# Performance work log

Measured on AMD Instinct MI355X. Metric: run time of the kernel, lower is better.

## Reference

```python
import jax, jax.numpy as jnp
import numpy as np

N, NPG, BS = 32000, 1000, 32
E, H, L, R, K = 512000, 128, 3, 8, 64


def setup_inputs() -> dict:
    key = jax.random.key(0)
    ks = jax.random.split(key, 16)
    sc = 0.05
    x = jax.random.normal(ks[0], (N, H), jnp.float32)
    W_rel = jax.random.normal(ks[1], (L, R, H, H), jnp.float32) * sc
    W_self = jax.random.normal(ks[2], (L, H, H), jnp.float32) * sc
    rel_table = jax.random.normal(ks[3], (R, H), jnp.float32)
    Zn = jax.random.normal(ks[4], (K, H), jnp.float32) * sc
    proj_W = jax.random.normal(ks[5], (L * H, H), jnp.float32) * sc
    proj_b = jnp.zeros((H,), jnp.float32)
    fc_W = jax.random.normal(ks[6], (2 * L * H + 2 * H, 1), jnp.float32) * sc
    fc_b = jnp.zeros((1,), jnp.float32)
    rep_seq = jax.random.normal(ks[7], (BS, H), jnp.float32)
    src = jax.random.randint(ks[8], (E,), 0, N, jnp.int32)
    dst = jax.random.randint(ks[9], (E,), 0, N, jnp.int32)
    etype = jax.random.randint(ks[10], (E,), 0, R, jnp.int32)
    graph_id = (jnp.arange(N, dtype=jnp.int32) // NPG).astype(jnp.int32)
    head_ids = (jnp.arange(BS, dtype=jnp.int32) * NPG)           # node with id==1 per subgraph
    tail_ids = (jnp.arange(BS, dtype=jnp.int32) * NPG + 1)       # node with id==2 per subgraph
    rel_labels = jax.random.randint(ks[11], (BS,), 0, R, jnp.int32)
    return dict(x=x, W_rel=W_rel, W_self=W_self, rel_table=rel_table, Zn=Zn,
                proj_W=proj_W, proj_b=proj_b, fc_W=fc_W, fc_b=fc_b, rep_seq=rep_seq,
                src=src, dst=dst, etype=etype, graph_id=graph_id,
                head_ids=head_ids, tail_ids=tail_ids, rel_labels=rel_labels)


def reference(x, W_rel, W_self, rel_table, Zn, proj_W, proj_b, fc_W, fc_b, rep_seq,
              src, dst, etype, graph_id, head_ids, tail_ids, rel_labels):
    n, h_dim = x.shape
    bs = head_ids.shape[0]
    # RGCN message passing: aggregate src features per (dst, rel), then per-rel linear.
    seg = dst.astype(jnp.int32) * R + etype.astype(jnp.int32)  # [E]
    h = x
    reprs = []
    for l in range(L):
        agg = jax.ops.segment_sum(h[src], seg, num_segments=n * R)  # [N*R, H]
        agg = agg.reshape(n, R, h_dim)
        msg = jnp.einsum('nri,rio->no', agg, W_rel[l])
        h = jax.nn.relu(msg + h @ W_self[l])
        reprs.append(h)
    repr_ = jnp.stack(reprs, axis=1)  # [N, L, H]
    # mean_nodes pooling per subgraph
    counts = jax.ops.segment_sum(jnp.ones((n,), x.dtype), graph_id, num_segments=bs)
    g_mean = jax.ops.segment_sum(repr_, graph_id, num_segments=bs) / counts[:, None, None]
    g_out = jax.nn.leaky_relu(g_mean.reshape(bs, L * h_dim) @ proj_W + proj_b)  # [bs, H]
    # head/tail gathers
    head_flat = repr_[head_ids].reshape(bs, L * h_dim)
    tail_flat = repr_[tail_ids].reshape(bs, L * h_dim)
    rel_embs = rel_table[rel_labels]  # [bs, H]
    h_out = head_flat @ proj_W + proj_b
    t_out = tail_flat @ proj_W + proj_b
    # community view: cluster assignment (softmax) then summary (sigmoid)
    s1 = jax.nn.sigmoid(jax.nn.softmax(h_out @ Zn.T, axis=-1) @ Zn)
    s2 = jax.nn.sigmoid(jax.nn.softmax(t_out @ Zn.T, axis=-1) @ Zn)
    s = s1 * s2
    # view attention aggregation over [subgraph, sequence, community] views
    views = jnp.stack([g_out, rep_seq, s], axis=1)  # [bs, 3, H]
    att = jax.nn.softmax(jnp.sum(rel_embs[:, None, :] * views, axis=-1), axis=-1)  # [bs, 3]
    view_aggr = jnp.sum(att[:, :, None] * views, axis=1)  # [bs, H]
    # positive triplet scoring
    g_rep = jnp.concatenate([head_flat, tail_flat, rel_embs, view_aggr], axis=1)
    out_pos = g_rep @ fc_W + fc_b  # [bs, 1]
    return out_pos
```

## Files before the change

kernel.cpp:

```cpp
#include <hip/hip_runtime.h>

#define N_NODES 32000
#define NPG     1000
#define BSZ     32
#define NEDGE   512000
#define H       128
#define NL      3
#define NR      8
#define NKK     1152
#define NKA     1024
#define NBIN2   262144

typedef __attribute__((ext_vector_type(8))) short short8;
typedef __attribute__((ext_vector_type(4))) float float4v;

__device__ __forceinline__ float bf2f(unsigned short u) {
  union { unsigned int i; float f; } v;
  v.i = ((unsigned int)u) << 16;
  return v.f;
}
__device__ __forceinline__ unsigned short f2bf(float f) {
  union { float f; unsigned int i; } v;
  v.f = f;
  unsigned int x = v.i;
  return (unsigned short)((x + 0x7FFFu + ((x >> 16) & 1u)) >> 16);
}

__device__ __forceinline__ void gl_lds16(const void* g, void* l) {
  __builtin_amdgcn_global_load_lds((__attribute__((address_space(1))) void*)g,
                                   (__attribute__((address_space(3))) void*)l,
                                   16, 0, 0);
}

__global__ __launch_bounds__(256) void k_prep(
    const float* __restrict__ x, const float* __restrict__ W_rel,
    const float* __restrict__ W_self, const int* __restrict__ dst,
    const int* __restrict__ etype, const int* __restrict__ graph_id,
    unsigned short* __restrict__ hb, unsigned short* __restrict__ Bt,
    int* __restrict__ cnt, int* __restrict__ gcount)
{
  const int b = blockIdx.x, t = threadIdx.x;
  if (b < 4000) {
    const size_t i = ((size_t)b * 256 + t) * 4;
    float4 v = *(const float4*)(x + i);
    ushort4 u = { f2bf(v.x), f2bf(v.y), f2bf(v.z), f2bf(v.w) };
    *(ushort4*)(hb + i) = u;
  } else if (b < 5728) {
    const int g = (b - 4000) * 256 + t;
    const int l = g / (H * NKK);
    const int rem = g - l * (H * NKK);
    const int o = rem / NKK;
    const int kk = rem - o * NKK;
    float v = (kk < 1024)
        ? W_rel[(((size_t)l * NR + (kk >> 7)) * H + (kk & 127)) * H + o]
        : W_self[((size_t)l * H + (kk - 1024)) * H + o];
    Bt[g] = f2bf(v);
  } else if (b < 7728) {
    const int e = (b - 5728) * 256 + t;
    atomicAdd(&cnt[dst[e] * 8 + etype[e]], 1);
  } else {
    __shared__ int hist[BSZ];
    if (t < BSZ) hist[t] = 0;
    __syncthreads();
    const int n = (b - 7728) * 256 + t;
    if (n < N_NODES) atomicAdd(&hist[graph_id[n]], 1);
    __syncthreads();
    if (t < BSZ) { int v = hist[t]; if (v) atomicAdd(&gcount[t], v); }
  }
}

__global__ __launch_bounds__(256) void k_scanA(const int* __restrict__ cnt,
                                               int* __restrict__ bsum) {
  __shared__ int red[256];
  const int t = threadIdx.x;
  int4 v = *(const int4*)(cnt + blockIdx.x * 1024 + t * 4);
  red[t] = v.x + v.y + v.z + v.w;
  __syncthreads();
  for (int off = 128; off > 0; off >>= 1) {
    if (t < off) red[t] += red[t + off];
    __syncthreads();
  }
  if (t == 0) bsum[blockIdx.x] = red[0];
}

__global__ __launch_bounds__(256) void k_scanC(const int* __restrict__ cnt,
                                               const int* __restrict__ bsum,
                                               int* __restrict__ row_ptr2,
                                               int* __restrict__ cursor) {
  __shared__ int ts[256], bsx[256];
  const int t = threadIdx.x;
  const int base = blockIdx.x * 1024 + t * 4;
  int4 v = *(const int4*)(cnt + base);
  const int s = v.x + v.y + v.z + v.w;
  ts[t]  = s;
  bsx[t] = bsum[t];
  __syncthreads();
  for (int off = 1; off < 256; off <<= 1) {
    int a = (t >= off) ? ts[t - off]  : 0;
    int c = (t >= off) ? bsx[t - off] : 0;
    __syncthreads();
    ts[t] += a; bsx[t] += c;
    __syncthreads();
  }
  const int boff = (blockIdx.x == 0) ? 0 : bsx[blockIdx.x - 1];
  int ex = ts[t] - s + boff;
  int4 w = { ex, ex + v.x, ex + v.x + v.y, ex + v.x + v.y + v.z };
  *(int4*)(row_ptr2 + base) = w;
  *(int4*)(cursor + base) = w;
}

__global__ void k_fill(const int* __restrict__ src, const int* __restrict__ dst,
                       const int* __restrict__ etype, int* __restrict__ cursor,
                       int* __restrict__ edge_off) {
  int e = blockIdx.x * blockDim.x + threadIdx.x;
  if (e < NEDGE) {
    int p = atomicAdd(&cursor[dst[e] * 8 + etype[e]], 1);
    edge_off[p] = src[e];
  }
}

__global__ __launch_bounds__(256) void k_agg(
    const unsigned short* __restrict__ Hin,
    const int* __restrict__ row_ptr2,
    const int* __restrict__ edge_off,
    unsigned short* __restrict__ A)
{
  const int tid = threadIdx.x;
  const int j  = tid >> 5;
  const int li = tid & 31;
  const int p  = li >> 4;
  const int q  = li & 15;
  const int n  = blockIdx.x;
  const uint4* H4 = (const uint4*)Hin;
  const int b = row_ptr2[n * 8 + j];
  const int e = row_ptr2[n * 8 + j + 1];
  float acc[8] = {0.f, 0.f, 0.f, 0.f, 0.f, 0.f, 0.f, 0.f};
#define ACC8(u, ok) { \
    const unsigned int xx = (ok) ? (u).x : 0u, yy = (ok) ? (u).y : 0u; \
    const unsigned int zz = (ok) ? (u).z : 0u, ww = (ok) ? (u).w : 0u; \
    acc[0] += bf2f((unsigned short)(xx & 0xffff)); \
    acc[1] += bf2f((unsigned short)(xx >> 16));    \
    acc[2] += bf2f((unsigned short)(yy & 0xffff)); \
    acc[3] += bf2f((unsigned short)(yy >> 16));    \
    acc[4] += bf2f((unsigned short)(zz & 0xffff)); \
    acc[5] += bf2f((unsigned short)(zz >> 16));    \
    acc[6] += bf2f((unsigned short)(ww & 0xffff)); \
    acc[7] += bf2f((unsigned short)(ww >> 16)); }
  for (int k = b + p; k < e; k += 4) {
    const int k1 = k + 2;
    const bool v1 = k1 < e;
    const int o0 = edge_off[k];
    const int o1 = edge_off[v1 ? k1 : k];
    uint4 u0 = H4[(size_t)o0 * 16 + q];
    uint4 u1 = H4[(size_t)o1 * 16 + q];
    ACC8(u0, true)
    ACC8(u1, v1)
  }
#undef ACC8
  #pragma unroll
  for (int i = 0; i < 8; ++i) acc[i] += __shfl_xor(acc[i], 16);
  if (p == 0) {
    uint4 w;
    w.x = (unsigned int)f2bf(acc[0]) | ((unsigned int)f2bf(acc[1]) << 16);
    w.y = (unsigned int)f2bf(acc[2]) | ((unsigned int)f2bf(acc[3]) << 16);
    w.z = (unsigned int)f2bf(acc[4]) | ((unsigned int)f2bf(acc[5]) << 16);
    w.w = (unsigned int)f2bf(acc[6]) | ((unsigned int)f2bf(acc[7]) << 16);
    *(uint4*)(A + (size_t)n * NKA + j * H + q * 8) = w;
  }
}

__global__ __launch_bounds__(256, 3) void k_gemmA(
    const unsigned short* __restrict__ Ag,
    const unsigned short* __restrict__ Bg,
    const unsigned short* __restrict__ Hin,
    unsigned short* __restrict__ Hout,
    float* __restrict__ gmean, int layer)
{
  __shared__ __align__(16) unsigned short pool[24576];
  const int tid = threadIdx.x;
  const int w = tid >> 6, lane = tid & 63;
  const int l15 = lane & 15, quad = lane >> 4;
  const int m0 = blockIdx.x * 64;
  const int rbase = (w & 1) * 32;
  const int cbase = (w >> 1) * 64;

  float4v acc[2][4];
  #pragma unroll
  for (int i = 0; i < 2; ++i)
    #pragma unroll
    for (int jj = 0; jj < 4; ++jj) acc[i][jj] = (float4v){0.f, 0.f, 0.f, 0.f};

  auto stageA = [&](unsigned short* dstL, const int kb) {
    #pragma unroll
    for (int rep = 0; rep < 2; ++rep) {
      const int g = rep * 256 + tid, row = g >> 3, c = g & 7;
      const unsigned short* srcp = (kb < NKA)
          ? Ag  + (size_t)(m0 + row) * NKA + kb + ((c ^ (row & 7)) * 8)
          : Hin + (size_t)(m0 + row) * H + (kb - NKA) + ((c ^ (row & 7)) * 8);
      gl_lds16(srcp, dstL + (size_t)g * 8);
    }
  };
  auto stageB = [&](unsigned short* dstL, const int kb) {
    #pragma unroll
    for (int rep = 0; rep < 4; ++rep) {
      const int g = rep * 256 + tid, row = g >> 3, c = g & 7;
      gl_lds16(Bg + (size_t)row * NKK + kb + ((c ^ (row & 7)) * 8), dstL + (size_t)g * 8);
    }
  };

  stageA(pool, 0);
  stageB(pool + 4096, 0);
  __syncthreads();

  #pragma unroll 2
  for (int kt = 0; kt < 18; ++kt) {
    const int cur = kt & 1;
    const unsigned short* ac = pool + (cur ? 12288 : 0);
    const unsigned short* bc = pool + (cur ? 16384 : 4096);
    if (kt < 17) {
      const int kb = (kt + 1) * 64;
      stageA(pool + (cur ? 0 : 12288), kb);
      stageB(pool + (cur ? 4096 : 16384), kb);
    }
    #pragma unroll
    for (int s = 0; s < 2; ++s) {
      const int c = s * 4 + quad;
      short8 af[2], bfv[4];
      #pragma unroll
      for (int i = 0; i < 2; ++i) {
        const int row = rbase + i * 16 + l15;
        af[i] = *(const short8*)(ac + row * 64 + ((c ^ (row & 7)) * 8));
      }
      #pragma unroll
      for (int jj = 0; jj < 4; ++jj) {
        const int orow = cbase + jj * 16 + l15;
        bfv[jj] = *(const short8*)(bc + orow * 64 + ((c ^ (orow & 7)) * 8));
      }
      #pragma unroll
      for (int i = 0; i < 2; ++i)
        #pragma unroll
        for (int jj = 0; jj < 4; ++jj)
          acc[i][jj] = __builtin_amdgcn_mfma_f32_16x16x32_bf16(af[i], bfv[jj], acc[i][jj], 0, 0, 0);
    }
    __syncthreads();
  }

  #pragma unroll
  for (int i = 0; i < 2; ++i)
    #pragma unroll
    for (int jj = 0; jj < 4; ++jj)
      #pragma unroll
      for (int r = 0; r < 4; ++r) {
        const int row = rbase + i * 16 + quad * 4 + r;
        const int col = cbase + jj * 16 + l15;
        pool[row * 136 + col] = f2bf(fmaxf(acc[i][jj][r], 0.f));
      }
  __syncthreads();
  #pragma unroll
  for (int rep = 0; rep < 4; ++rep) {
    const int g = rep * 256 + tid;
    const int row = g >> 4, c = g & 15;
    *(uint4*)(Hout + (size_t)(m0 + row) * H + c * 8) = *(const uint4*)(pool + row * 136 + c * 8);
  }

  const int g0 = m0 / NPG;
  const int bnd = (g0 + 1) * NPG - m0;
  if (tid < H) {
    float s0 = 0.f, s1 = 0.f;
    #pragma unroll 8
    for (int r2 = 0; r2 < 64; ++r2) {
      float v = bf2f(pool[r2 * 136 + tid]);
      if (r2 < bnd) s0 += v; else s1 += v;
    }
    atomicAdd(&gmean[(size_t)g0 * (NL * H) + layer * H + tid], s0);
    if (bnd < 64)
      atomicAdd(&gmean[(size_t)(g0 + 1) * (NL * H) + layer * H + tid], s1);
  }
}

__global__ __launch_bounds__(128) void k_final(
    const unsigned short* __restrict__ hb, const float* __restrict__ gmean,
    const int* __restrict__ gcount,
    const float* __restrict__ rel_tb, const float* __restrict__ Zn,
    const float* __restrict__ projW, const float* __restrict__ projB,
    const float* __restrict__ fcW, const float* __restrict__ fcB,
    const float* __restrict__ repSeq,
    const int* __restrict__ head_ids, const int* __restrict__ tail_ids,
    const int* __restrict__ rel_lab, float* __restrict__ out)
{
  const int b = blockIdx.x;
  const int o = threadIdx.x;
  __shared__ float gm[384], hf[384], tf[384];
  __shared__ float go[128], ho[128], t_o[128], re[128], rs[128], sv[128];
  __shared__ float lg[128], pr[128], red[128], att[3];

  const int hid = head_ids[b], tlid = tail_ids[b], rl = rel_lab[b];
  const float cinv = 1.f / (float)gcount[b];
  #pragma unroll
  for (int l = 0; l < NL; ++l) {
    gm[l * H + o] = gmean[(size_t)b * (NL * H) + l * H + o] * cinv;
    hf[l * H + o] = bf2f(hb[((size_t)(l + 1) * N_NODES + hid) * H + o]);
    tf[l * H + o] = bf2f(hb[((size_t)(l + 1) * N_NODES + tlid) * H + o]);
  }
  re[o] = rel_tb[rl * H + o];
  rs[o] = repSeq[b * H + o];
  __syncthreads();

  float pb = projB[o];
  float sg = pb, sh = pb, st = pb;
  for (int i = 0; i < NL * H; ++i) {
    float wv = projW[i * H + o];
    sg = fmaf(gm[i], wv, sg);
    sh = fmaf(hf[i], wv, sh);
    st = fmaf(tf[i], wv, st);
  }
  go[o] = (sg > 0.f) ? sg : 0.01f * sg;
  ho[o] = sh;
  t_o[o] = st;
  __syncthreads();

  {
    const int k = o & 63;
    const float* v = (o < 64) ? ho : t_o;
    float s = 0.f;
    for (int i = 0; i < H; ++i) s = fmaf(v[i], Zn[k * H + i], s);
    lg[o] = s;
  }
  __syncthreads();
  if (o < 2) {
    float* l0 = &lg[o * 64];
    float* p0 = &pr[o * 64];
    float mx = l0[0];
    for (int k = 1; k < 64; ++k) mx = fmaxf(mx, l0[k]);
    float sum = 0.f;
    for (int k = 0; k < 64; ++k) { float e = __expf(l0[k] - mx); p0[k] = e; sum += e; }
    float inv = 1.f / sum;
    for (int k = 0; k < 64; ++k) p0[k] *= inv;
  }
  __syncthreads();
  {
    float s1 = 0.f, s2 = 0.f;
    for (int k = 0; k < 64; ++k) {
      float z = Zn[k * H + o];
      s1 = fmaf(pr[k], z, s1);
      s2 = fmaf(pr[64 + k], z, s2);
    }
    s1 = 1.f / (1.f + __expf(-s1));
    s2 = 1.f / (1.f + __expf(-s2));
    sv[o] = s1 * s2;
  }
  __syncthreads();
  if (o == 0) {
    float d0 = 0.f, d1 = 0.f, d2 = 0.f;
    for (int i = 0; i < H; ++i) { d0 += re[i] * go[i]; d1 += re[i] * rs[i]; d2 += re[i] * sv[i]; }
    float mx = fmaxf(d0, fmaxf(d1, d2));
    float e0 = __expf(d0 - mx), e1 = __expf(d1 - mx), e2 = __expf(d2 - mx);
    float inv = 1.f / (e0 + e1 + e2);
    att[0] = e0 * inv; att[1] = e1 * inv; att[2] = e2 * inv;
  }
  __syncthreads();
  float va = att[0] * go[o] + att[1] * rs[o] + att[2] * sv[o];

  float p = 0.f;
  p = fmaf(hf[o],       fcW[o],       p);
  p = fmaf(hf[128 + o], fcW[128 + o], p);
  p = fmaf(hf[256 + o], fcW[256 + o], p);
  p = fmaf(tf[o],       fcW[384 + o], p);
  p = fmaf(tf[128 + o], fcW[512 + o], p);
  p = fmaf(tf[256 + o], fcW[640 + o], p);
  p = fmaf(re[o],       fcW[768 + o], p);
  p = fmaf(va,          fcW[896 + o], p);
  red[o] = p;
  __syncthreads();
  if (o == 0) {
    float s = 0.f;
    for (int i = 0; i < 128; ++i) s += red[i];
    out[b] = s + fcB[0];
  }
}

extern "C" void kernel_launch(void* const* d_in, const int* in_sizes, int n_in,
                              void* d_out, int out_size, void* d_ws, size_t ws_size,
                              hipStream_t stream) {
  const float* x        = (const float*)d_in[0];
  const float* W_rel    = (const float*)d_in[1];
  const float* W_self   = (const float*)d_in[2];
  const float* rel_tb   = (const float*)d_in[3];
  const float* Zn       = (const float*)d_in[4];
  const float* proj_W   = (const float*)d_in[5];
  const float* proj_b   = (const float*)d_in[6];
  const float* fc_W     = (const float*)d_in[7];
  const float* fc_b     = (const float*)d_in[8];
  const float* rep_seq  = (const float*)d_in[9];
  const int* src      = (const int*)d_in[10];
  const int* dst      = (const int*)d_in[11];
  const int* etype    = (const int*)d_in[12];
  const int* graph_id = (const int*)d_in[13];
  const int* head_ids = (const int*)d_in[14];
  const int* tail_ids = (const int*)d_in[15];
  const int* rel_lab  = (const int*)d_in[16];
  float* out = (float*)d_out;

  char* w = (char*)d_ws;
  unsigned short* A   = (unsigned short*)w; w += (size_t)N_NODES * NKA * 2;
  unsigned short* hb  = (unsigned short*)w; w += (size_t)(NL + 1) * N_NODES * H * 2;
  unsigned short* Bt2 = (unsigned short*)w; w += (size_t)NL * H * NKK * 2;
  int* row_ptr2 = (int*)w;  w += (size_t)(NBIN2 + 8) * 4;
  int* cursor   = (int*)w;  w += (size_t)NBIN2 * 4;
  int* edge_off = (int*)w;  w += (size_t)NEDGE * 4;
  int* bsum     = (int*)w;  w += (size_t)256 * 4;
  char* z = w;
  int* cnt     = (int*)w;   w += (size_t)NBIN2 * 4;
  int* gcount  = (int*)w;   w += (size_t)32 * 4;
  float* gmean = (float*)w; w += (size_t)BSZ * NL * H * 4;
  size_t zbytes = (size_t)(w - z);

  hipMemsetAsync(z, 0, zbytes, stream);
  k_prep <<<7853, 256, 0, stream>>>(x, W_rel, W_self, dst, etype, graph_id, hb, Bt2, cnt, gcount);
  k_scanA<<<NBIN2 / 1024, 256, 0, stream>>>(cnt, bsum);
  k_scanC<<<NBIN2 / 1024, 256, 0, stream>>>(cnt, bsum, row_ptr2, cursor);
  k_fill <<<NEDGE / 256, 256, 0, stream>>>(src, dst, etype, cursor, edge_off);

  for (int l = 0; l < NL; ++l) {
    const unsigned short* hp = hb + (size_t)l * N_NODES * H;
    unsigned short* hn = hb + (size_t)(l + 1) * N_NODES * H;
    k_agg  <<<N_NODES, 256, 0, stream>>>(hp, row_ptr2, edge_off, A);
    k_gemmA<<<N_NODES / 64, 256, 0, stream>>>(A, Bt2 + (size_t)l * H * NKK, hp, hn, gmean, l);
  }
  k_final<<<BSZ, H, 0, stream>>>(hb, gmean, gcount, rel_tb, Zn, proj_W, proj_b, fc_W, fc_b,
                                 rep_seq, head_ids, tail_ids, rel_lab, out);
  (void)in_sizes; (void)n_in; (void)out_size; (void)ws_size;
}
```

Baseline: 333.3 us.

## Triple-buffer gemmA LDS pipeline with explicit vmcnt waits and nontemporal stores

Converts the k_gemmA main loop from double-buffered to triple-buffered LDS staging, prefetching two K-tiles ahead and using explicit s_waitcnt vmcnt counts with raw s_barrier instead of __syncthreads. This is meant to hide global-to-LDS load latency behind MFMA work. It raises LDS use to 72KB per block and lowers launch bounds occupancy from 3 to 2 blocks per CU. The aggregation kernel's output store also becomes a nontemporal vector store to reduce cache pollution.

Result: slower. 346.4 us (+3.9%).

```diff
diff --git a/kernel.cpp b/kernel.cpp
--- a/kernel.cpp
+++ b/kernel.cpp
@@ -13,6 +13,7 @@
 
 typedef __attribute__((ext_vector_type(8))) short short8;
 typedef __attribute__((ext_vector_type(4))) float float4v;
+typedef __attribute__((ext_vector_type(4))) unsigned int uint4v;
 
 __device__ __forceinline__ float bf2f(unsigned short u) {
   union { unsigned int i; float f; } v;
@@ -160,23 +161,23 @@
   #pragma unroll
   for (int i = 0; i < 8; ++i) acc[i] += __shfl_xor(acc[i], 16);
   if (p == 0) {
-    uint4 w;
-    w.x = (unsigned int)f2bf(acc[0]) | ((unsigned int)f2bf(acc[1]) << 16);
-    w.y = (unsigned int)f2bf(acc[2]) | ((unsigned int)f2bf(acc[3]) << 16);
-    w.z = (unsigned int)f2bf(acc[4]) | ((unsigned int)f2bf(acc[5]) << 16);
-    w.w = (unsigned int)f2bf(acc[6]) | ((unsigned int)f2bf(acc[7]) << 16);
-    *(uint4*)(A + (size_t)n * NKA + j * H + q * 8) = w;
-  }
-}
-
-__global__ __launch_bounds__(256, 3) void k_gemmA(
+    uint4v w = {
+      (unsigned int)f2bf(acc[0]) | ((unsigned int)f2bf(acc[1]) << 16),
+      (unsigned int)f2bf(acc[2]) | ((unsigned int)f2bf(acc[3]) << 16),
+      (unsigned int)f2bf(acc[4]) | ((unsigned int)f2bf(acc[5]) << 16),
+      (unsigned int)f2bf(acc[6]) | ((unsigned int)f2bf(acc[7]) << 16) };
+    __builtin_nontemporal_store(w, (uint4v*)(A + (size_t)n * NKA + j * H + q * 8));
+  }
+}
+
+__global__ __launch_bounds__(256, 2) void k_gemmA(
     const unsigned short* __restrict__ Ag,
     const unsigned short* __restrict__ Bg,
     const unsigned short* __restrict__ Hin,
     unsigned short* __restrict__ Hout,
     float* __restrict__ gmean, int layer)
 {
-  __shared__ __align__(16) unsigned short pool[24576];
+  __shared__ __align__(16) unsigned short pool[36864];
   const int tid = threadIdx.x;
   const int w = tid >> 6, lane = tid & 63;
   const int l15 = lane & 15, quad = lane >> 4;
@@ -207,21 +208,7 @@
       gl_lds16(Bg + (size_t)row * NKK + kb + ((c ^ (row & 7)) * 8), dstL + (size_t)g * 8);
     }
   };
-
-  stageA(pool, 0);
-  stageB(pool + 4096, 0);
-  __syncthreads();
-
-  #pragma unroll 2
-  for (int kt = 0; kt < 18; ++kt) {
-    const int cur = kt & 1;
-    const unsigned short* ac = pool + (cur ? 12288 : 0);
-    const unsigned short* bc = pool + (cur ? 16384 : 4096);
-    if (kt < 17) {
-      const int kb = (kt + 1) * 64;
-      stageA(pool + (cur ? 0 : 12288), kb);
-      stageB(pool + (cur ? 4096 : 16384), kb);
-    }
+  auto compute = [&](const unsigned short* ac, const unsigned short* bc) {
     #pragma unroll
     for (int s = 0; s < 2; ++s) {
       const int c = s * 4 + quad;
@@ -242,8 +229,35 @@
         for (int jj = 0; jj < 4; ++jj)
           acc[i][jj] = __builtin_amdgcn_mfma_f32_16x16x32_bf16(af[i], bfv[jj], acc[i][jj], 0, 0, 0);
     }
-    __syncthreads();
-  }
+  };
+
+#define STEP(KT, CUR, NXT)                                              \
+  {                                                                     \
+    if ((KT) + 2 < 18) {                                                \
+      stageA(pool + (NXT), ((KT) + 2) * 64);                            \
+      stageB(pool + (NXT) + 4096, ((KT) + 2) * 64);                     \
+      asm volatile("s_waitcnt vmcnt(12)" ::: "memory");                 \
+    } else if ((KT) + 1 < 18) {                                         \
+      asm volatile("s_waitcnt vmcnt(6)" ::: "memory");                  \
+    } else {                                                            \
+      asm volatile("s_waitcnt vmcnt(0)" ::: "memory");                  \
+    }                                                                   \
+    __builtin_amdgcn_s_barrier();                                       \
+    __builtin_amdgcn_sched_barrier(0);                                  \
+    compute(pool + (CUR), pool + (CUR) + 4096);                         \
+    __builtin_amdgcn_sched_barrier(0);                                  \
+    __builtin_amdgcn_s_barrier();                                       \
+  }
+
+  stageA(pool, 0);            stageB(pool + 4096, 0);
+  stageA(pool + 12288, 64);   stageB(pool + 12288 + 4096, 64);
+
+  for (int kt = 0; kt < 18; kt += 3) {
+    STEP(kt,     0,     24576);
+    STEP(kt + 1, 12288, 0);
+    STEP(kt + 2, 24576, 12288);
+  }
+#undef STEP
 
   #pragma unroll
   for (int i = 0; i < 2; ++i)
```
